# Optimization experiments

Measured on AMD Instinct MI355X. Metric: run time of the kernel, lower is better.

The kernel has to match this reference:

```python
import jax, jax.numpy as jnp
import numpy as np

N, E = 20000, 100000
D_IN, H1, C1 = 512, 8, 64   # conv1: 512 -> 8 heads x 64, concat -> 512
H2, C2 = 4, 128             # conv2: 512 -> 4 heads x 128, mean -> 128


def setup_inputs() -> dict:
    key = jax.random.key(0)
    k = jax.random.split(key, 12)
    s_in = 1.0 / np.sqrt(D_IN).astype(np.float32)
    return {
        "street_embedding": jax.random.normal(k[0], (N, D_IN), jnp.float32),
        "edge_index": jax.random.randint(k[1], (2, E), 0, N),
        "y": jax.random.randint(k[2], (N,), 0, C2),
        "train_mask": jax.random.bernoulli(k[3], 0.5, (N,)),
        "W1": jax.random.normal(k[4], (D_IN, H1 * C1), jnp.float32) * s_in,
        "att_src1": jax.random.normal(k[5], (H1, C1), jnp.float32) * 0.1,
        "att_dst1": jax.random.normal(k[6], (H1, C1), jnp.float32) * 0.1,
        "b1": jnp.zeros((H1 * C1,), jnp.float32),
        "W2": jax.random.normal(k[7], (H1 * C1, H2 * C2), jnp.float32) * s_in,
        "att_src2": jax.random.normal(k[8], (H2, C2), jnp.float32) * 0.1,
        "att_dst2": jax.random.normal(k[9], (H2, C2), jnp.float32) * 0.1,
        "b2": jnp.zeros((C2,), jnp.float32),
    }


def _gat_conv(x, W, a_src, a_dst, b, src, dst, n, H, C, concat):
    # linear transform (no bias, as in PyG GATConv's internal lin)
    xp = (x @ W).reshape(n, H, C)                      # [N,H,C]
    asrc = jnp.einsum('nhc,hc->nh', xp, a_src)         # [N,H]
    adst = jnp.einsum('nhc,hc->nh', xp, a_dst)
    e = jax.nn.leaky_relu(asrc[src] + adst[dst], 0.2)  # [E',H] edge scores
    # softmax over incoming edges per destination node
    m = jax.lax.stop_gradient(jax.ops.segment_max(e, dst, num_segments=n))
    ex = jnp.exp(e - m[dst])
    denom = jax.ops.segment_sum(ex, dst, num_segments=n)
    alpha = ex / (denom[dst] + 1e-16)                  # [E',H]
    out = jax.ops.segment_sum(alpha[:, :, None] * xp[src], dst, num_segments=n)  # [N,H,C]
    if concat:
        return out.reshape(n, H * C) + b
    return out.mean(axis=1) + b


def reference(street_embedding, edge_index, y, train_mask,
              W1, att_src1, att_dst1, b1, W2, att_src2, att_dst2, b2):
    n = street_embedding.shape[0]
    loop = jnp.arange(n)
    # PyG GATConv adds self-loops by default
    src = jnp.concatenate([edge_index[0], loop])
    dst = jnp.concatenate([edge_index[1], loop])
    # dropout layers are identity in eval mode
    h = _gat_conv(street_embedding, W1, att_src1, att_dst1, b1, src, dst, n, H1, C1, True)
    h = jax.nn.elu(h)
    out = _gat_conv(h, W2, att_src2, att_dst2, b2, src, dst, n, H2, C2, False)  # [N,C2]
    # CrossEntropyLoss, mean over train_mask nodes (weighted mean, jit-safe)
    logp = jax.nn.log_softmax(out, axis=-1)
    ce = -jnp.take_along_axis(logp, y[:, None], axis=-1)[:, 0]
    w = train_mask.astype(out.dtype)
    loss_su = jnp.sum(w * ce) / jnp.sum(w)
    return (loss_su, out)
```

## Files before the change

### kernel.cpp

```cpp
#include <hip/hip_runtime.h>
#include <cmath>

#define D_IN 512
#define HC   512
#define NH1  8
#define NC1  64
#define NH2  4
#define NC2  128
#define BM 128
#define BN 128
#define BK 64

typedef __attribute__((ext_vector_type(8))) short short8;
typedef __attribute__((ext_vector_type(8))) unsigned short u16x8;
typedef __attribute__((ext_vector_type(8))) unsigned short ushort8;
typedef __attribute__((ext_vector_type(4))) float f32x4;

__device__ inline ushort f2bf(float f) {
  unsigned u = __float_as_uint(f);
  return (ushort)((u + 0x7FFFu + ((u >> 16) & 1u)) >> 16);
}
__device__ inline float bf2f(ushort b) { return __uint_as_float(((unsigned)b) << 16); }

__global__ void k_pre(const float* __restrict__ x, ushort* __restrict__ Abf,
                      const float* __restrict__ W1, const float* __restrict__ W2,
                      ushort* __restrict__ Wt1, ushort* __restrict__ Wt2, int n4x,
                      const int* __restrict__ ei, int E, int Etot,
                      int* __restrict__ cnt) {
  __shared__ float tl[64][65];
  int t = threadIdx.x;
  int bx = blockIdx.x;
  int nxb = (n4x + 255) >> 8;
  if (bx < nxb) {
    int i = bx * 256 + t;
    if (i < n4x) {
      float4 v = ((const float4*)x)[i];
      ushort4 r = { f2bf(v.x), f2bf(v.y), f2bf(v.z), f2bf(v.w) };
      ((ushort4*)Abf)[i] = r;
    }
  } else if (bx < nxb + 128) {
    int b = bx - nxb;
    int w = b >> 6, tile = b & 63;
    int k0 = (tile >> 3) * 64, n0 = (tile & 7) * 64;
    const float* W = w ? W2 : W1;
    ushort* Wt = w ? Wt2 : Wt1;
    int r = t >> 2, q = t & 3;
    const float4* src = (const float4*)(W + (size_t)(k0 + r) * HC + n0 + q * 16);
#pragma unroll
    for (int j = 0; j < 4; ++j) {
      float4 v = src[j];
      tl[r][q * 16 + 4 * j + 0] = v.x;
      tl[r][q * 16 + 4 * j + 1] = v.y;
      tl[r][q * 16 + 4 * j + 2] = v.z;
      tl[r][q * 16 + 4 * j + 3] = v.w;
    }
    __syncthreads();
    ushort8* dst = (ushort8*)(Wt + (size_t)(n0 + r) * D_IN + k0 + q * 16);
#pragma unroll
    for (int j = 0; j < 2; ++j) {
      ushort8 o;
#pragma unroll
      for (int c = 0; c < 8; ++c) o[c] = f2bf(tl[q * 16 + 8 * j + c][r]);
      dst[j] = o;
    }
  } else {
    int e = (bx - nxb - 128) * 256 + t;
    if (e >= Etot) return;
    int d = (e < E) ? ei[E + e] : e - E;
    atomicAdd(&cnt[d], 1);
  }
}

template<int H, int SCAN>
__global__ void k_gemm_bf16(const ushort* __restrict__ A, const ushort* __restrict__ Bt,
                            ushort* __restrict__ Cbf,
                            const float* __restrict__ att_s, const float* __restrict__ att_d,
                            float* __restrict__ asrc, float* __restrict__ adst, int M,
                            const int* __restrict__ cnt, int* __restrict__ rowstart, int Nn) {
  constexpr int C = HC / H;
  __shared__ __align__(16) ushort As[BM * BK];
  __shared__ __align__(16) ushort Bs[BN * BK];
  int t = threadIdx.x;

  if (SCAN && blockIdx.x == 0) {
    int* sA = (int*)As;
    int* sB = (int*)Bs;
    int lane = t & 63, w = t >> 6;
    const int4* c4 = (const int4*)cnt;
    int nb4 = (Nn + 3) >> 2;
    int T4 = (nb4 + 255) >> 8;
    if (T4 <= 20) {
      for (int i = 0; i < T4; ++i) {
        int g = i * 256 + t;
        int s = 0;
        if (g < nb4) { int4 v = c4[g]; s = v.x + v.y + v.z + v.w; }
        (g < 4096 ? sA[g] : sB[g - 4096]) = s;
      }
      __syncthreads();
      int base = t * T4;
      int S = 0;
      for (int i = 0; i < T4; ++i) {
        int g = base + i;
        if (g < nb4) S += (g < 4096 ? sA[g] : sB[g - 4096]);
      }
      int v = S;
#pragma unroll
      for (int off = 1; off < 64; off <<= 1) {
        int u = __shfl_up(v, off);
        if (lane >= off) v += u;
      }
      if (lane == 63) sB[3000 + w] = v;
      __syncthreads();
      int wp = 0;
#pragma unroll
      for (int i = 0; i < 4; ++i) if (i < w) wp += sB[3000 + i];
      int run = wp + v - S;
      for (int i = 0; i < T4; ++i) {
        int g = base + i;
        if (g < nb4) {
          int c = (g < 4096 ? sA[g] : sB[g - 4096]);
          (g < 4096 ? sA[g] : sB[g - 4096]) = run;
          run += c;
        }
      }
      __syncthreads();
      for (int i = 0; i < T4; ++i) {
        int g = i * 256 + t;
        if (g < nb4) {
          int4 v = c4[g];
          int p = (g < 4096 ? sA[g] : sB[g - 4096]);
          int jb = g * 4;
          if (jb + 0 < Nn) rowstart[jb + 0] = p;  p += v.x;
          if (jb + 1 < Nn) rowstart[jb + 1] = p;  p += v.y;
          if (jb + 2 < Nn) rowstart[jb + 2] = p;  p += v.z;
          if (jb + 3 < Nn) rowstart[jb + 3] = p;  p += v.w;
          if (jb + 4 >= Nn) rowstart[Nn] = p;
        }
      }
    } else {
      int T = (Nn + 255) / 256;
      int base = t * T;
      int sum = 0;
      for (int i = 0; i < T; ++i) { int j = base + i; if (j < Nn) sum += cnt[j]; }
      int v = sum;
#pragma unroll
      for (int off = 1; off < 64; off <<= 1) {
        int u = __shfl_up(v, off);
        if (lane >= off) v += u;
      }
      if (lane == 63) sB[3000 + w] = v;
      __syncthreads();
      int wp = 0;
#pragma unroll
      for (int i = 0; i < 4; ++i) if (i < w) wp += sB[3000 + i];
      int run = wp + v - sum;
      for (int i = 0; i < T; ++i) {
        int j = base + i;
        if (j < Nn) { rowstart[j] = run; run += cnt[j]; }
      }
      if (t == 255) rowstart[Nn] = run;
    }
    return;
  }

  int lin = blockIdx.x - (SCAN ? 1 : 0);
  int nwg = gridDim.x - (SCAN ? 1 : 0);
  int q = nwg >> 3, r = nwg & 7;
  int xcd = lin & 7, pos = lin >> 3;
  int wg = (xcd < r ? xcd * (q + 1) : r * (q + 1) + (xcd - r) * q) + pos;
  int m0 = (wg >> 2) * BM;
  int n0 = (wg & 3) * BN;

  int wave = t >> 6, lane = t & 63;
  int ln = lane & 15, qd = lane >> 4;
  int wm = (wave >> 1) * 64, wn = (wave & 1) * 64;

  f32x4 acc[4][4] = {};

  int g = t >> 6, ct = (t >> 4) & 3, lt = t & 15;
  int rA0 = m0 + g * 16 + lt;      if (rA0 > M - 1) rA0 = M - 1;
  int rA1 = m0 + 64 + g * 16 + lt; if (rA1 > M - 1) rA1 = M - 1;
  const ushort* gA0 = A + (size_t)rA0 * D_IN + ct * 8;
  const ushort* gA1 = A + (size_t)rA1 * D_IN + ct * 8;
  const ushort* gB0 = Bt + (size_t)(n0 + g * 16 + lt) * D_IN + ct * 8;
  const ushort* gB1 = Bt + (size_t)(n0 + 64 + g * 16 + lt) * D_IN + ct * 8;

  for (int k0 = 0; k0 < D_IN; k0 += BK) {
    __syncthreads();
#pragma unroll
    for (int h = 0; h < 2; ++h) {
      int ko = k0 + h * 32;
      int lo = h * 4096;
      __builtin_amdgcn_global_load_lds(
          (const __attribute__((address_space(1))) void*)(gA0 + ko),
          (__attribute__((address_space(3))) void*)(As + lo + t * 8), 16, 0, 0);
      __builtin_amdgcn_global_load_lds(
          (const __attribute__((address_space(1))) void*)(gA1 + ko),
          (__attribute__((address_space(3))) void*)(As + lo + 2048 + t * 8), 16, 0, 0);
      __builtin_amdgcn_global_load_lds(
          (const __attribute__((address_space(1))) void*)(gB0 + ko),
          (__attribute__((address_space(3))) void*)(Bs + lo + t * 8), 16, 0, 0);
      __builtin_amdgcn_global_load_lds(
          (const __attribute__((address_space(1))) void*)(gB1 + ko),
          (__attribute__((address_space(3))) void*)(Bs + lo + 2048 + t * 8), 16, 0, 0);
    }
    __syncthreads();
#pragma unroll
    for (int h = 0; h < 2; ++h) {
      int lo = h * 4096;
      short8 a[4], bb[4];
#pragma unroll
      for (int i = 0; i < 4; ++i)
        a[i] = *(const short8*)&As[lo + (((wave >> 1) * 4 + i) * 4 + qd) * 128 + ln * 8];
#pragma unroll
      for (int j = 0; j < 4; ++j)
        bb[j] = *(const short8*)&Bs[lo + (((wave & 1) * 4 + j) * 4 + qd) * 128 + ln * 8];
#pragma unroll
      for (int i = 0; i < 4; ++i)
#pragma unroll
        for (int j = 0; j < 4; ++j)
          acc[i][j] = __builtin_amdgcn_mfma_f32_16x16x32_bf16(a[i], bb[j], acc[i][j], 0, 0, 0);
    }
  }

#pragma unroll
  for (int i = 0; i < 4; ++i) {
#pragma unroll
    for (int reg = 0; reg < 4; ++reg) {
      int row = m0 + wm + i * 16 + qd * 4 + reg;
      if (row >= M) continue;
#pragma unroll
      for (int j = 0; j < 4; ++j)
        Cbf[(size_t)row * HC + n0 + wn + j * 16 + ln] = f2bf(acc[i][j][reg]);
    }
  }

  int colbase = n0 + wn;
  int h = colbase / C;
  float sa[4], da[4];
#pragma unroll
  for (int j = 0; j < 4; ++j) {
    int c = (colbase % C) + j * 16 + ln;
    sa[j] = att_s[h * C + c];
    da[j] = att_d[h * C + c];
  }
#pragma unroll
  for (int i = 0; i < 4; ++i) {
#pragma unroll
    for (int reg = 0; reg < 4; ++reg) {
      float ps = acc[i][0][reg] * sa[0] + acc[i][1][reg] * sa[1]
               + acc[i][2][reg] * sa[2] + acc[i][3][reg] * sa[3];
      float pd = acc[i][0][reg] * da[0] + acc[i][1][reg] * da[1]
               + acc[i][2][reg] * da[2] + acc[i][3][reg] * da[3];
#pragma unroll
      for (int o = 1; o < 16; o <<= 1) { ps += __shfl_xor(ps, o); pd += __shfl_xor(pd, o); }
      int row = m0 + wm + i * 16 + qd * 4 + reg;
      if (ln == 0 && row < M) {
        if (C == 64) {
          asrc[row * H + h] = ps; adst[row * H + h] = pd;
        } else {
          int sub = (colbase >> 6) & 1;
          asrc[(row * H + h) * 2 + sub] = ps;
          adst[(row * H + h) * 2 + sub] = pd;
        }
      }
    }
  }
}

__global__ void k_scatter(const int* __restrict__ ei, int E, int Etot,
                          const int* __restrict__ rowstart, int* __restrict__ cursor,
                          int* __restrict__ csr_src) {
  int e = blockIdx.x * blockDim.x + threadIdx.x;
  if (e >= Etot) return;
  int s = (e < E) ? ei[e] : e - E;
  int d = (e < E) ? ei[E + e] : e - E;
  int pos = atomicAdd(&cursor[d], 1);
  csr_src[rowstart[d] + pos] = s;
}

template<int H, int MODE>
__global__ void k_agg(const int* __restrict__ rowstart, const int* __restrict__ csr_src,
                      const float* __restrict__ asrc, const float* __restrict__ adst,
                      const ushort* __restrict__ xp, ushort* __restrict__ hout,
                      float* __restrict__ out2, const float* __restrict__ bias,
                      const int* __restrict__ y, const int* __restrict__ msk,
                      float* __restrict__ acc2, int N) {
  int wv = threadIdx.x >> 6, lane = threadIdx.x & 63;
  int n = blockIdx.x * 4 + wv;
  if (n >= N) return;
  int h = (MODE == 1) ? (lane >> 3) : (lane >> 4);
  int beg = rowstart[n], end = rowstart[n + 1];

  float adn;
  if (MODE == 1) adn = adst[n * H + h];
  else { float2 t2 = ((const float2*)adst)[n * H + h]; adn = t2.x + t2.y; }

  float acc[8] = {};
  float wsum = 0.f;

#define SCR(s_)  ((MODE == 1) ? asrc[(s_) * H + h] \
                   : (((const float2*)asrc)[(s_) * H + h].x + \
                      ((const float2*)asrc)[(s_) * H + h].y))
#define EDGE(w_, a_)  do {                                   \
    float ww = (w_);                                         \
    _Pragma("unroll") for (int k = 0; k < 8; ++k)            \
      acc[k] += ww * bf2f((a_)[k]);                          \
    wsum += ww; } while (0)
#define LRELU(v_) ((v_) > 0.f ? (v_) : 0.2f * (v_))

  for (int c0 = beg; c0 < end; c0 += 64) {
    int len = end - c0; if (len > 64) len = 64;
    int ev = (lane < len) ? csr_src[c0 + lane] : 0;
    int j = 0;
    for (; j + 3 < len; j += 4) {
      int s0 = __shfl(ev, j), s1 = __shfl(ev, j + 1);
      int s2 = __shfl(ev, j + 2), s3 = __shfl(ev, j + 3);
      float v0 = SCR(s0) + adn, v1 = SCR(s1) + adn;
      float v2 = SCR(s2) + adn, v3 = SCR(s3) + adn;
      u16x8 a0 = ((const u16x8*)xp)[(size_t)s0 * 64 + lane];
      u16x8 a1 = ((const u16x8*)xp)[(size_t)s1 * 64 + lane];
      u16x8 a2 = ((const u16x8*)xp)[(size_t)s2 * 64 + lane];
      u16x8 a3 = ((const u16x8*)xp)[(size_t)s3 * 64 + lane];
      EDGE(__expf(LRELU(v0)), a0);
      EDGE(__expf(LRELU(v1)), a1);
      EDGE(__expf(LRELU(v2)), a2);
      EDGE(__expf(LRELU(v3)), a3);
    }
    for (; j + 1 < len; j += 2) {
      int s0 = __shfl(ev, j), s1 = __shfl(ev, j + 1);
      float v0 = SCR(s0) + adn, v1 = SCR(s1) + adn;
      u16x8 a0 = ((const u16x8*)xp)[(size_t)s0 * 64 + lane];
      u16x8 a1 = ((const u16x8*)xp)[(size_t)s1 * 64 + lane];
      EDGE(__expf(LRELU(v0)), a0);
      EDGE(__expf(LRELU(v1)), a1);
    }
    if (j < len) {
      int s0 = __shfl(ev, j);
      float v0 = SCR(s0) + adn;
      u16x8 a0 = ((const u16x8*)xp)[(size_t)s0 * 64 + lane];
      EDGE(__expf(LRELU(v0)), a0);
    }
  }
#undef SCR
#undef EDGE
#undef LRELU

  float rdn = 1.0f / (wsum + 1e-16f);
#pragma unroll
  for (int k = 0; k < 8; ++k) acc[k] *= rdn;

  if (MODE == 1) {
    int c = lane * 8;
    u16x8 rr;
#pragma unroll
    for (int k = 0; k < 8; ++k) {
      float v = acc[k] + bias[c + k];
      v = (v > 0.f) ? v : expm1f(v);
      rr[k] = f2bf(v);
    }
    ((u16x8*)hout)[(size_t)n * 64 + lane] = rr;
  } else {
#pragma unroll
    for (int k = 0; k < 8; ++k) {
      float v = acc[k];
      v += __shfl_xor(v, 16);
      v += __shfl_xor(v, 32);
      acc[k] = v * 0.25f + bias[(lane & 15) * 8 + k];
    }
    if (lane < 16) {
      int cb = lane * 8;
#pragma unroll
      for (int k = 0; k < 8; ++k) out2[(size_t)n * NC2 + cb + k] = acc[k];
    }
    float mx = acc[0];
#pragma unroll
    for (int k = 1; k < 8; ++k) mx = fmaxf(mx, acc[k]);
#pragma unroll
    for (int o = 1; o < 16; o <<= 1) mx = fmaxf(mx, __shfl_xor(mx, o));
    float e = 0.f;
#pragma unroll
    for (int k = 0; k < 8; ++k) e += __expf(acc[k] - mx);
#pragma unroll
    for (int o = 1; o < 16; o <<= 1) e += __shfl_xor(e, o);
    int yv = y[n];
    float sel = acc[0];
#pragma unroll
    for (int k = 1; k < 8; ++k) sel = ((yv & 7) == k) ? acc[k] : sel;
    float vy = __shfl(sel, yv >> 3);
    if (lane == 0 && msk[n] != 0) {
      float ce = mx + logf(e) - vy;
      int slot = n & 127;
      atomicAdd(&acc2[slot], ce);
      atomicAdd(&acc2[128 + slot], 1.0f);
    }
  }
}

__global__ void k_final(const float* __restrict__ acc2, float* __restrict__ out0) {
  int tid = threadIdx.x;
  float ce = acc2[tid], ct = acc2[128 + tid];
#pragma unroll
  for (int o = 32; o > 0; o >>= 1) { ce += __shfl_xor(ce, o); ct += __shfl_xor(ct, o); }
  __shared__ float s[4];
  if ((tid & 63) == 0) { s[(tid >> 6) * 2] = ce; s[(tid >> 6) * 2 + 1] = ct; }
  __syncthreads();
  if (tid == 0) out0[0] = (s[0] + s[2]) / (s[1] + s[3]);
}

extern "C" void kernel_launch(void* const* d_in, const int* in_sizes, int n_in,
                              void* d_out, int out_size, void* d_ws, size_t ws_size,
                              hipStream_t stream) {
  const float* x   = (const float*)d_in[0];
  const int*   ei  = (const int*)d_in[1];
  const int*   y   = (const int*)d_in[2];
  const int*   msk = (const int*)d_in[3];
  const float* W1  = (const float*)d_in[4];
  const float* as1 = (const float*)d_in[5];
  const float* ad1 = (const float*)d_in[6];
  const float* b1  = (const float*)d_in[7];
  const float* W2  = (const float*)d_in[8];
  const float* as2 = (const float*)d_in[9];
  const float* ad2 = (const float*)d_in[10];
  const float* b2  = (const float*)d_in[11];
  float* out = (float*)d_out;

  int N = in_sizes[0] / D_IN;
  int E = in_sizes[1] / 2;
  int Etot = E + N;

  float* ws = (float*)d_ws;
  size_t NF = (size_t)N * HC;
  float* asr1 = ws;
  float* adt1 = asr1 + (size_t)N * NH1;
  float* asr2 = adt1 + (size_t)N * NH1;
  float* adt2 = asr2 + (size_t)N * 2 * NH2;
  float* acc2 = adt2 + (size_t)N * 2 * NH2;
  int*   cnt    = (int*)(acc2 + 256);
  int*   cursor = cnt + N;
  size_t zero_bytes = (256 + 2 * (size_t)N) * sizeof(float);
  int*   rowstart = cursor + N;
  int*   csr_src  = rowstart + N + 1;
  ushort* xpbf = (ushort*)((((uintptr_t)(csr_src + Etot)) + 15) & ~(uintptr_t)15);
  ushort* Abf = xpbf + NF;
  ushort* Wt1 = Abf + NF;
  ushort* Wt2 = Wt1 + (size_t)D_IN * HC;

  hipMemsetAsync(acc2, 0, zero_bytes, stream);

  int n4x = (int)(NF / 4);
  int nxb = (n4x + 255) / 256;
  int nhb = (Etot + 255) / 256;
  k_pre<<<nxb + 128 + nhb, 256, 0, stream>>>(x, Abf, W1, W2, Wt1, Wt2, n4x,
                                             ei, E, Etot, cnt);

  int nwg = (HC / BN) * ((N + BM - 1) / BM);
  int aggblocks = (N + 3) / 4;

  k_gemm_bf16<NH1, 1><<<nwg + 1, 256, 0, stream>>>(Abf, Wt1, xpbf, as1, ad1, asr1, adt1, N,
                                                   cnt, rowstart, N);
  k_scatter<<<(Etot + 255) / 256, 256, 0, stream>>>(ei, E, Etot, rowstart, cursor, csr_src);
  k_agg<NH1, 1><<<aggblocks, 256, 0, stream>>>(rowstart, csr_src, asr1, adt1, xpbf, Abf,
                                               nullptr, b1, nullptr, nullptr, nullptr, N);

  k_gemm_bf16<NH2, 0><<<nwg, 256, 0, stream>>>(Abf, Wt2, xpbf, as2, ad2, asr2, adt2, N,
                                               nullptr, nullptr, N);
  k_agg<NH2, 2><<<aggblocks, 256, 0, stream>>>(rowstart, csr_src, asr2, adt2, xpbf, nullptr,
                                               out + 1, b2, y, msk, acc2, N);

  k_final<<<1, 128, 0, stream>>>(acc2, out);
}
```

Baseline: 268.0 us.

## Split layer-1 aggregation per head with head-major attention scores

Layer-1 aggregation now launches one block per head slice (8x blocks). In each wave, 8 lane groups each take a different edge and each lane covers 8 channels of a single head, with a cross-group shuffle reduction at the end. The attention score arrays for layer 1 are stored head-major, so per-head score gathers read a contiguous array. blockIdx&7 picks the head, so consecutive blocks handle different heads of the same nodes, which is meant to raise parallelism and shrink each gather to 16 bytes per lane. The cost is more blocks, repeated reads of the CSR for every head, and extra shuffle reductions.

```diff
diff --git a/kernel.cpp b/kernel.cpp
--- a/kernel.cpp
+++ b/kernel.cpp
@@ -257,7 +257,8 @@
       int row = m0 + wm + i * 16 + qd * 4 + reg;
       if (ln == 0 && row < M) {
         if (C == 64) {
-          asrc[row * H + h] = ps; adst[row * H + h] = pd;
+          asrc[(size_t)h * M + row] = ps;
+          adst[(size_t)h * M + row] = pd;
         } else {
           int sub = (colbase >> 6) & 1;
           asrc[(row * H + h) * 2 + sub] = ps;
@@ -279,29 +280,78 @@
   csr_src[rowstart[d] + pos] = s;
 }
 
-template<int H, int MODE>
-__global__ void k_agg(const int* __restrict__ rowstart, const int* __restrict__ csr_src,
-                      const float* __restrict__ asrc, const float* __restrict__ adst,
-                      const ushort* __restrict__ xp, ushort* __restrict__ hout,
-                      float* __restrict__ out2, const float* __restrict__ bias,
-                      const int* __restrict__ y, const int* __restrict__ msk,
-                      float* __restrict__ acc2, int N) {
+__global__ void k_agg1(const int* __restrict__ rowstart, const int* __restrict__ csr_src,
+                       const float* __restrict__ asrc, const float* __restrict__ adst,
+                       const ushort* __restrict__ xp, ushort* __restrict__ hout,
+                       const float* __restrict__ bias, int N) {
+  int wv = threadIdx.x >> 6, lane = threadIdx.x & 63;
+  int s = blockIdx.x & 7;
+  int n = (blockIdx.x >> 3) * 4 + wv;
+  if (n >= N) return;
+  int grp = lane >> 3, li = lane & 7;
+  int beg = rowstart[n], end = rowstart[n + 1];
+  float adn = adst[(size_t)s * N + n];
+  const float* as_s = asrc + (size_t)s * N;
+  const ushort* xs = xp + s * NC1 + li * 8;
+
+  float acc[8] = {};
+  float wsum = 0.f;
+  for (int c0 = beg; c0 < end; c0 += 64) {
+    int len = end - c0; if (len > 64) len = 64;
+    int ev = (lane < len) ? csr_src[c0 + lane] : 0;
+    for (int j = 0; j < len; j += 8) {
+      int idx = j + grp;
+      bool val = idx < len;
+      int src = __shfl(ev, val ? idx : 0);
+      float v = as_s[src] + adn;
+      v = (v > 0.f) ? v : 0.2f * v;
+      float w = val ? __expf(v) : 0.f;
+      u16x8 a = *(const u16x8*)(xs + (size_t)src * HC);
+#pragma unroll
+      for (int k = 0; k < 8; ++k) acc[k] += w * bf2f(a[k]);
+      wsum += w;
+    }
+  }
+#pragma unroll
+  for (int o = 8; o < 64; o <<= 1) {
+    wsum += __shfl_xor(wsum, o);
+#pragma unroll
+    for (int k = 0; k < 8; ++k) acc[k] += __shfl_xor(acc[k], o);
+  }
+  if (grp == 0) {
+    float rdn = 1.0f / (wsum + 1e-16f);
+    u16x8 rr;
+#pragma unroll
+    for (int k = 0; k < 8; ++k) {
+      float v = acc[k] * rdn + bias[s * NC1 + li * 8 + k];
+      v = (v > 0.f) ? v : expm1f(v);
+      rr[k] = f2bf(v);
+    }
+    __builtin_nontemporal_store(rr, (u16x8*)(hout + (size_t)n * HC + s * NC1 + li * 8));
+  }
+}
+
+__global__ void k_agg2(const int* __restrict__ rowstart, const int* __restrict__ csr_src,
+                       const float* __restrict__ asrc, const float* __restrict__ adst,
+                       const ushort* __restrict__ xp,
+                       float* __restrict__ out2, const float* __restrict__ bias,
+                       const int* __restrict__ y, const int* __restrict__ msk,
+                       float* __restrict__ acc2, int N) {
+  constexpr int H = NH2;
   int wv = threadIdx.x >> 6, lane = threadIdx.x & 63;
   int n = blockIdx.x * 4 + wv;
   if (n >= N) return;
-  int h = (MODE == 1) ? (lane >> 3) : (lane >> 4);
+  int h = lane >> 4;
   int beg = rowstart[n], end = rowstart[n + 1];
 
-  float adn;
-  if (MODE == 1) adn = adst[n * H + h];
-  else { float2 t2 = ((const float2*)adst)[n * H + h]; adn = t2.x + t2.y; }
+  float2 t2 = ((const float2*)adst)[n * H + h];
+  float adn = t2.x + t2.y;
 
   float acc[8] = {};
   float wsum = 0.f;
 
-#define SCR(s_)  ((MODE == 1) ? asrc[(s_) * H + h] \
-                   : (((const float2*)asrc)[(s_) * H + h].x + \
-                      ((const float2*)asrc)[(s_) * H + h].y))
+#define SCR(s_)  (((const float2*)asrc)[(s_) * H + h].x + \
+                  ((const float2*)asrc)[(s_) * H + h].y)
 #define EDGE(w_, a_)  do {                                   \
     float ww = (w_);                                         \
     _Pragma("unroll") for (int k = 0; k < 8; ++k)            \
@@ -350,50 +400,38 @@
 #pragma unroll
   for (int k = 0; k < 8; ++k) acc[k] *= rdn;
 
-  if (MODE == 1) {
-    int c = lane * 8;
-    u16x8 rr;
-#pragma unroll
-    for (int k = 0; k < 8; ++k) {
-      float v = acc[k] + bias[c + k];
-      v = (v > 0.f) ? v : expm1f(v);
-      rr[k] = f2bf(v);
-    }
-    ((u16x8*)hout)[(size_t)n * 64 + lane] = rr;
-  } else {
-#pragma unroll
-    for (int k = 0; k < 8; ++k) {
-      float v = acc[k];
-      v += __shfl_xor(v, 16);
-      v += __shfl_xor(v, 32);
-      acc[k] = v * 0.25f + bias[(lane & 15) * 8 + k];
-    }
-    if (lane < 16) {
-      int cb = lane * 8;
-#pragma unroll
-      for (int k = 0; k < 8; ++k) out2[(size_t)n * NC2 + cb + k] = acc[k];
-    }
-    float mx = acc[0];
-#pragma unroll
-    for (int k = 1; k < 8; ++k) mx = fmaxf(mx, acc[k]);
-#pragma unroll
-    for (int o = 1; o < 16; o <<= 1) mx = fmaxf(mx, __shfl_xor(mx, o));
-    float e = 0.f;
-#pragma unroll
-    for (int k = 0; k < 8; ++k) e += __expf(acc[k] - mx);
-#pragma unroll
-    for (int o = 1; o < 16; o <<= 1) e += __shfl_xor(e, o);
-    int yv = y[n];
-    float sel = acc[0];
-#pragma unroll
-    for (int k = 1; k < 8; ++k) sel = ((yv & 7) == k) ? acc[k] : sel;
-    float vy = __shfl(sel, yv >> 3);
-    if (lane == 0 && msk[n] != 0) {
-      float ce = mx + logf(e) - vy;
-      int slot = n & 127;
-      atomicAdd(&acc2[slot], ce);
-      atomicAdd(&acc2[128 + slot], 1.0f);
-    }
+#pragma unroll
+  for (int k = 0; k < 8; ++k) {
+    float v = acc[k];
+    v += __shfl_xor(v, 16);
+    v += __shfl_xor(v, 32);
+    acc[k] = v * 0.25f + bias[(lane & 15) * 8 + k];
+  }
+  if (lane < 16) {
+    int cb = lane * 8;
+#pragma unroll
+    for (int k = 0; k < 8; ++k) out2[(size_t)n * NC2 + cb + k] = acc[k];
+  }
+  float mx = acc[0];
+#pragma unroll
+  for (int k = 1; k < 8; ++k) mx = fmaxf(mx, acc[k]);
+#pragma unroll
+  for (int o = 1; o < 16; o <<= 1) mx = fmaxf(mx, __shfl_xor(mx, o));
+  float e = 0.f;
+#pragma unroll
+  for (int k = 0; k < 8; ++k) e += __expf(acc[k] - mx);
+#pragma unroll
+  for (int o = 1; o < 16; o <<= 1) e += __shfl_xor(e, o);
+  int yv = y[n];
+  float sel = acc[0];
+#pragma unroll
+  for (int k = 1; k < 8; ++k) sel = ((yv & 7) == k) ? acc[k] : sel;
+  float vy = __shfl(sel, yv >> 3);
+  if (lane == 0 && msk[n] != 0) {
+    float ce = mx + logf(e) - vy;
+    int slot = n & 127;
+    atomicAdd(&acc2[slot], ce);
+    atomicAdd(&acc2[128 + slot], 1.0f);
   }
 }
 
@@ -455,18 +493,18 @@
                                              ei, E, Etot, cnt);
 
   int nwg = (HC / BN) * ((N + BM - 1) / BM);
-  int aggblocks = (N + 3) / 4;
+  int agg1blocks = 8 * ((N + 3) / 4);
+  int agg2blocks = (N + 3) / 4;
 
   k_gemm_bf16<NH1, 1><<<nwg + 1, 256, 0, stream>>>(Abf, Wt1, xpbf, as1, ad1, asr1, adt1, N,
                                                    cnt, rowstart, N);
   k_scatter<<<(Etot + 255) / 256, 256, 0, stream>>>(ei, E, Etot, rowstart, cursor, csr_src);
-  k_agg<NH1, 1><<<aggblocks, 256, 0, stream>>>(rowstart, csr_src, asr1, adt1, xpbf, Abf,
-                                               nullptr, b1, nullptr, nullptr, nullptr, N);
+  k_agg1<<<agg1blocks, 256, 0, stream>>>(rowstart, csr_src, asr1, adt1, xpbf, Abf, b1, N);
 
   k_gemm_bf16<NH2, 0><<<nwg, 256, 0, stream>>>(Abf, Wt2, xpbf, as2, ad2, asr2, adt2, N,
                                                nullptr, nullptr, N);
-  k_agg<NH2, 2><<<aggblocks, 256, 0, stream>>>(rowstart, csr_src, asr2, adt2, xpbf, nullptr,
-                                               out + 1, b2, y, msk, acc2, N);
+  k_agg2<<<agg2blocks, 256, 0, stream>>>(rowstart, csr_src, asr2, adt2, xpbf,
+                                         out + 1, b2, y, msk, acc2, N);
 
   k_final<<<1, 128, 0, stream>>>(acc2, out);
 }
```

Result: slower. 331.5 us (+23.7%).

## Fuse edge scatter into GEMM launch and final loss reduction into last agg block

Applied to the files above, without the earlier changes.

The CSR scatter kernel is folded into the first GEMM launch as extra blocks that spin-wait on a global flag set by the scan block. The separate final-reduction kernel is replaced by a last-block-done pattern inside the second aggregation kernel, using an atomic counter. This removes two kernel launches and lets the scatter overlap with the GEMM, at the cost of spin-waiting blocks that may occupy CUs, and it relies on the scan block being scheduled before the waiting blocks to avoid deadlock.

```diff
diff --git a/kernel.cpp b/kernel.cpp
--- a/kernel.cpp
+++ b/kernel.cpp
@@ -76,11 +76,15 @@
                             ushort* __restrict__ Cbf,
                             const float* __restrict__ att_s, const float* __restrict__ att_d,
                             float* __restrict__ asrc, float* __restrict__ adst, int M,
-                            const int* __restrict__ cnt, int* __restrict__ rowstart, int Nn) {
+                            const int* __restrict__ cnt, int* __restrict__ rowstart, int Nn,
+                            const int* __restrict__ ei, int E, int Etot,
+                            int* __restrict__ cursor, int* __restrict__ csr_src,
+                            int* __restrict__ syncv) {
   constexpr int C = HC / H;
   __shared__ __align__(16) ushort As[BM * BK];
   __shared__ __align__(16) ushort Bs[BN * BK];
   int t = threadIdx.x;
+  int nwg = ((M + BM - 1) / BM) * (HC / BN);
 
   if (SCAN && blockIdx.x == 0) {
     int* sA = (int*)As;
@@ -160,11 +164,26 @@
       }
       if (t == 255) rowstart[Nn] = run;
     }
+    __syncthreads();
+    if (t == 0) { __threadfence(); atomicAdd(&syncv[0], 1); }
     return;
   }
 
+  if (SCAN && blockIdx.x > nwg) {
+    if (t == 0) { while (atomicAdd(&syncv[0], 0) == 0) __builtin_amdgcn_s_sleep(8); }
+    __syncthreads();
+    __threadfence();
+    int e = (blockIdx.x - nwg - 1) * 256 + t;
+    if (e < Etot) {
+      int s = (e < E) ? ei[e] : e - E;
+      int d = (e < E) ? ei[E + e] : e - E;
+      int pos = atomicAdd(&cursor[d], 1);
+      csr_src[rowstart[d] + pos] = s;
+    }
+    return;
+  }
+
   int lin = blockIdx.x - (SCAN ? 1 : 0);
-  int nwg = gridDim.x - (SCAN ? 1 : 0);
   int q = nwg >> 3, r = nwg & 7;
   int xcd = lin & 7, pos = lin >> 3;
   int wg = (xcd < r ? xcd * (q + 1) : r * (q + 1) + (xcd - r) * q) + pos;
@@ -268,36 +287,29 @@
   }
 }
 
-__global__ void k_scatter(const int* __restrict__ ei, int E, int Etot,
-                          const int* __restrict__ rowstart, int* __restrict__ cursor,
-                          int* __restrict__ csr_src) {
-  int e = blockIdx.x * blockDim.x + threadIdx.x;
-  if (e >= Etot) return;
-  int s = (e < E) ? ei[e] : e - E;
-  int d = (e < E) ? ei[E + e] : e - E;
-  int pos = atomicAdd(&cursor[d], 1);
-  csr_src[rowstart[d] + pos] = s;
-}
-
 template<int H, int MODE>
 __global__ void k_agg(const int* __restrict__ rowstart, const int* __restrict__ csr_src,
                       const float* __restrict__ asrc, const float* __restrict__ adst,
                       const ushort* __restrict__ xp, ushort* __restrict__ hout,
                       float* __restrict__ out2, const float* __restrict__ bias,
                       const int* __restrict__ y, const int* __restrict__ msk,
-                      float* __restrict__ acc2, int N) {
+                      float* __restrict__ acc2, int N,
+                      float* __restrict__ out0, int* __restrict__ syncv) {
   int wv = threadIdx.x >> 6, lane = threadIdx.x & 63;
   int n = blockIdx.x * 4 + wv;
-  if (n >= N) return;
-  int h = (MODE == 1) ? (lane >> 3) : (lane >> 4);
-  int beg = rowstart[n], end = rowstart[n + 1];
-
-  float adn;
-  if (MODE == 1) adn = adst[n * H + h];
-  else { float2 t2 = ((const float2*)adst)[n * H + h]; adn = t2.x + t2.y; }
-
-  float acc[8] = {};
-  float wsum = 0.f;
+  if (MODE == 1 && n >= N) return;
+  bool act = (n < N);
+
+  if (act) {
+    int h = (MODE == 1) ? (lane >> 3) : (lane >> 4);
+    int beg = rowstart[n], end = rowstart[n + 1];
+
+    float adn;
+    if (MODE == 1) adn = adst[n * H + h];
+    else { float2 t2 = ((const float2*)adst)[n * H + h]; adn = t2.x + t2.y; }
+
+    float acc[8] = {};
+    float wsum = 0.f;
 
 #define SCR(s_)  ((MODE == 1) ? asrc[(s_) * H + h] \
                    : (((const float2*)asrc)[(s_) * H + h].x + \
@@ -309,103 +321,116 @@
     wsum += ww; } while (0)
 #define LRELU(v_) ((v_) > 0.f ? (v_) : 0.2f * (v_))
 
-  for (int c0 = beg; c0 < end; c0 += 64) {
-    int len = end - c0; if (len > 64) len = 64;
-    int ev = (lane < len) ? csr_src[c0 + lane] : 0;
-    int j = 0;
-    for (; j + 3 < len; j += 4) {
-      int s0 = __shfl(ev, j), s1 = __shfl(ev, j + 1);
-      int s2 = __shfl(ev, j + 2), s3 = __shfl(ev, j + 3);
-      float v0 = SCR(s0) + adn, v1 = SCR(s1) + adn;
-      float v2 = SCR(s2) + adn, v3 = SCR(s3) + adn;
-      u16x8 a0 = ((const u16x8*)xp)[(size_t)s0 * 64 + lane];
-      u16x8 a1 = ((const u16x8*)xp)[(size_t)s1 * 64 + lane];
-      u16x8 a2 = ((const u16x8*)xp)[(size_t)s2 * 64 + lane];
-      u16x8 a3 = ((const u16x8*)xp)[(size_t)s3 * 64 + lane];
-      EDGE(__expf(LRELU(v0)), a0);
-      EDGE(__expf(LRELU(v1)), a1);
-      EDGE(__expf(LRELU(v2)), a2);
-      EDGE(__expf(LRELU(v3)), a3);
-    }
-    for (; j + 1 < len; j += 2) {
-      int s0 = __shfl(ev, j), s1 = __shfl(ev, j + 1);
-      float v0 = SCR(s0) + adn, v1 = SCR(s1) + adn;
-      u16x8 a0 = ((const u16x8*)xp)[(size_t)s0 * 64 + lane];
-      u16x8 a1 = ((const u16x8*)xp)[(size_t)s1 * 64 + lane];
-      EDGE(__expf(LRELU(v0)), a0);
-      EDGE(__expf(LRELU(v1)), a1);
-    }
-    if (j < len) {
-      int s0 = __shfl(ev, j);
-      float v0 = SCR(s0) + adn;
-      u16x8 a0 = ((const u16x8*)xp)[(size_t)s0 * 64 + lane];
-      EDGE(__expf(LRELU(v0)), a0);
-    }
-  }
+    for (int c0 = beg; c0 < end; c0 += 64) {
+      int len = end - c0; if (len > 64) len = 64;
+      int ev = (lane < len) ? csr_src[c0 + lane] : 0;
+      int j = 0;
+      for (; j + 3 < len; j += 4) {
+        int s0 = __shfl(ev, j), s1 = __shfl(ev, j + 1);
+        int s2 = __shfl(ev, j + 2), s3 = __shfl(ev, j + 3);
+        float v0 = SCR(s0) + adn, v1 = SCR(s1) + adn;
+        float v2 = SCR(s2) + adn, v3 = SCR(s3) + adn;
+        u16x8 a0 = ((const u16x8*)xp)[(size_t)s0 * 64 + lane];
+        u16x8 a1 = ((const u16x8*)xp)[(size_t)s1 * 64 + lane];
+        u16x8 a2 = ((const u16x8*)xp)[(size_t)s2 * 64 + lane];
+        u16x8 a3 = ((const u16x8*)xp)[(size_t)s3 * 64 + lane];
+        EDGE(__expf(LRELU(v0)), a0);
+        EDGE(__expf(LRELU(v1)), a1);
+        EDGE(__expf(LRELU(v2)), a2);
+        EDGE(__expf(LRELU(v3)), a3);
+      }
+      for (; j + 1 < len; j += 2) {
+        int s0 = __shfl(ev, j), s1 = __shfl(ev, j + 1);
+        float v0 = SCR(s0) + adn, v1 = SCR(s1) + adn;
+        u16x8 a0 = ((const u16x8*)xp)[(size_t)s0 * 64 + lane];
+        u16x8 a1 = ((const u16x8*)xp)[(size_t)s1 * 64 + lane];
+        EDGE(__expf(LRELU(v0)), a0);
+        EDGE(__expf(LRELU(v1)), a1);
+      }
+      if (j < len) {
+        int s0 = __shfl(ev, j);
+        float v0 = SCR(s0) + adn;
+        u16x8 a0 = ((const u16x8*)xp)[(size_t)s0 * 64 + lane];
+        EDGE(__expf(LRELU(v0)), a0);
+      }
+    }
 #undef SCR
 #undef EDGE
 #undef LRELU
 
-  float rdn = 1.0f / (wsum + 1e-16f);
-#pragma unroll
-  for (int k = 0; k < 8; ++k) acc[k] *= rdn;
-
-  if (MODE == 1) {
-    int c = lane * 8;
-    u16x8 rr;
-#pragma unroll
-    for (int k = 0; k < 8; ++k) {
-      float v = acc[k] + bias[c + k];
-      v = (v > 0.f) ? v : expm1f(v);
-      rr[k] = f2bf(v);
-    }
-    ((u16x8*)hout)[(size_t)n * 64 + lane] = rr;
-  } else {
-#pragma unroll
-    for (int k = 0; k < 8; ++k) {
-      float v = acc[k];
-      v += __shfl_xor(v, 16);
-      v += __shfl_xor(v, 32);
-      acc[k] = v * 0.25f + bias[(lane & 15) * 8 + k];
-    }
-    if (lane < 16) {
-      int cb = lane * 8;
-#pragma unroll
-      for (int k = 0; k < 8; ++k) out2[(size_t)n * NC2 + cb + k] = acc[k];
-    }
-    float mx = acc[0];
-#pragma unroll
-    for (int k = 1; k < 8; ++k) mx = fmaxf(mx, acc[k]);
-#pragma unroll
-    for (int o = 1; o < 16; o <<= 1) mx = fmaxf(mx, __shfl_xor(mx, o));
-    float e = 0.f;
-#pragma unroll
-    for (int k = 0; k < 8; ++k) e += __expf(acc[k] - mx);
-#pragma unroll
-    for (int o = 1; o < 16; o <<= 1) e += __shfl_xor(e, o);
-    int yv = y[n];
-    float sel = acc[0];
-#pragma unroll
-    for (int k = 1; k < 8; ++k) sel = ((yv & 7) == k) ? acc[k] : sel;
-    float vy = __shfl(sel, yv >> 3);
-    if (lane == 0 && msk[n] != 0) {
-      float ce = mx + logf(e) - vy;
-      int slot = n & 127;
-      atomicAdd(&acc2[slot], ce);
-      atomicAdd(&acc2[128 + slot], 1.0f);
-    }
-  }
-}
-
-__global__ void k_final(const float* __restrict__ acc2, float* __restrict__ out0) {
-  int tid = threadIdx.x;
-  float ce = acc2[tid], ct = acc2[128 + tid];
-#pragma unroll
-  for (int o = 32; o > 0; o >>= 1) { ce += __shfl_xor(ce, o); ct += __shfl_xor(ct, o); }
-  __shared__ float s[4];
-  if ((tid & 63) == 0) { s[(tid >> 6) * 2] = ce; s[(tid >> 6) * 2 + 1] = ct; }
-  __syncthreads();
-  if (tid == 0) out0[0] = (s[0] + s[2]) / (s[1] + s[3]);
+    float rdn = 1.0f / (wsum + 1e-16f);
+#pragma unroll
+    for (int k = 0; k < 8; ++k) acc[k] *= rdn;
+
+    if (MODE == 1) {
+      int c = lane * 8;
+      u16x8 rr;
+#pragma unroll
+      for (int k = 0; k < 8; ++k) {
+        float v = acc[k] + bias[c + k];
+        v = (v > 0.f) ? v : expm1f(v);
+        rr[k] = f2bf(v);
+      }
+      ((u16x8*)hout)[(size_t)n * 64 + lane] = rr;
+    } else {
+#pragma unroll
+      for (int k = 0; k < 8; ++k) {
+        float v = acc[k];
+        v += __shfl_xor(v, 16);
+        v += __shfl_xor(v, 32);
+        acc[k] = v * 0.25f + bias[(lane & 15) * 8 + k];
+      }
+      if (lane < 16) {
+        int cb = lane * 8;
+#pragma unroll
+        for (int k = 0; k < 8; ++k) out2[(size_t)n * NC2 + cb + k] = acc[k];
+      }
+      float mx = acc[0];
+#pragma unroll
+      for (int k = 1; k < 8; ++k) mx = fmaxf(mx, acc[k]);
+#pragma unroll
+      for (int o = 1; o < 16; o <<= 1) mx = fmaxf(mx, __shfl_xor(mx, o));
+      float e = 0.f;
+#pragma unroll
+      for (int k = 0; k < 8; ++k) e += __expf(acc[k] - mx);
+#pragma unroll
+      for (int o = 1; o < 16; o <<= 1) e += __shfl_xor(e, o);
+      int yv = y[n];
+      float sel = acc[0];
+#pragma unroll
+      for (int k = 1; k < 8; ++k) sel = ((yv & 7) == k) ? acc[k] : sel;
+      float vy = __shfl(sel, yv >> 3);
+      if (lane == 0 && msk[n] != 0) {
+        float ce = mx + logf(e) - vy;
+        int slot = n & 127;
+        atomicAdd(&acc2[slot], ce);
+        atomicAdd(&acc2[128 + slot], 1.0f);
+      }
+    }
+  }
+
+  if (MODE == 2) {
+    __shared__ int s_last;
+    __shared__ float sred[4];
+    __syncthreads();
+    if (threadIdx.x == 0) {
+      __threadfence();
+      s_last = (atomicAdd(&syncv[1], 1) == (int)gridDim.x - 1) ? 1 : 0;
+    }
+    __syncthreads();
+    if (s_last) {
+      int tid = threadIdx.x;
+      if (tid < 128) {
+        float ce = atomicAdd(&acc2[tid], 0.0f);
+        float ct = atomicAdd(&acc2[128 + tid], 0.0f);
+#pragma unroll
+        for (int o = 32; o > 0; o >>= 1) { ce += __shfl_xor(ce, o); ct += __shfl_xor(ct, o); }
+        if ((tid & 63) == 0) { sred[(tid >> 6) * 2] = ce; sred[(tid >> 6) * 2 + 1] = ct; }
+      }
+      __syncthreads();
+      if (threadIdx.x == 0) out0[0] = (sred[0] + sred[2]) / (sred[1] + sred[3]);
+    }
+  }
 }
 
 extern "C" void kernel_launch(void* const* d_in, const int* in_sizes, int n_in,
@@ -436,9 +461,10 @@
   float* asr2 = adt1 + (size_t)N * NH1;
   float* adt2 = asr2 + (size_t)N * 2 * NH2;
   float* acc2 = adt2 + (size_t)N * 2 * NH2;
-  int*   cnt    = (int*)(acc2 + 256);
+  int*   syncv  = (int*)(acc2 + 256);
+  int*   cnt    = syncv + 16;
   int*   cursor = cnt + N;
-  size_t zero_bytes = (256 + 2 * (size_t)N) * sizeof(float);
+  size_t zero_bytes = (256 + 16 + 2 * (size_t)N) * sizeof(float);
   int*   rowstart = cursor + N;
   int*   csr_src  = rowstart + N + 1;
   ushort* xpbf = (ushort*)((((uintptr_t)(csr_src + Etot)) + 15) & ~(uintptr_t)15);
@@ -455,18 +481,20 @@
                                              ei, E, Etot, cnt);
 
   int nwg = (HC / BN) * ((N + BM - 1) / BM);
+  int nscat = (Etot + 255) / 256;
   int aggblocks = (N + 3) / 4;
 
-  k_gemm_bf16<NH1, 1><<<nwg + 1, 256, 0, stream>>>(Abf, Wt1, xpbf, as1, ad1, asr1, adt1, N,
-                                                   cnt, rowstart, N);
-  k_scatter<<<(Etot + 255) / 256, 256, 0, stream>>>(ei, E, Etot, rowstart, cursor, csr_src);
+  k_gemm_bf16<NH1, 1><<<1 + nwg + nscat, 256, 0, stream>>>(
+      Abf, Wt1, xpbf, as1, ad1, asr1, adt1, N,
+      cnt, rowstart, N, ei, E, Etot, cursor, csr_src, syncv);
   k_agg<NH1, 1><<<aggblocks, 256, 0, stream>>>(rowstart, csr_src, asr1, adt1, xpbf, Abf,
-                                               nullptr, b1, nullptr, nullptr, nullptr, N);
-
-  k_gemm_bf16<NH2, 0><<<nwg, 256, 0, stream>>>(Abf, Wt2, xpbf, as2, ad2, asr2, adt2, N,
-                                               nullptr, nullptr, N);
+                                               nullptr, b1, nullptr, nullptr, nullptr, N,
+                                               nullptr, nullptr);
+
+  k_gemm_bf16<NH2, 0><<<nwg, 256, 0, stream>>>(
+      Abf, Wt2, xpbf, as2, ad2, asr2, adt2, N,
+      nullptr, nullptr, N, nullptr, 0, 0, nullptr, nullptr, nullptr);
   k_agg<NH2, 2><<<aggblocks, 256, 0, stream>>>(rowstart, csr_src, asr2, adt2, xpbf, nullptr,
-                                               out + 1, b2, y, msk, acc2, N);
-
-  k_final<<<1, 128, 0, stream>>>(acc2, out);
+                                               out + 1, b2, y, msk, acc2, N,
+                                               out, syncv);
 }
```

Measured after the change: 429.7 us. 60.4% more time.
